# Optimization experiments

Hardware: AMD Instinct MI355X
Metric: run time of the kernel (lower is better)

The kernel has to match this reference:

```python
import jax, jax.numpy as jnp
import numpy as np

N_NODES = 10000
N_EDGES = 100000
DIM = 768
NEG_SLOPE = 0.2  # PyG GATConv default


def gat_conv(x, src, dst, W, att_src, att_dst, bias, num_nodes):
    """Single-head PyG-style GATConv. src/dst already include self-loops."""
    h = x @ W                                  # [N, D]
    a_s = h @ att_src                          # [N]
    a_d = h @ att_dst                          # [N]
    e = jax.nn.leaky_relu(a_s[src] + a_d[dst], NEG_SLOPE)  # [E']
    # segment softmax over edges sharing the same destination node
    m = jax.ops.segment_max(e, dst, num_segments=num_nodes)  # [N]
    e = jnp.exp(e - m[dst])
    denom = jax.ops.segment_sum(e, dst, num_segments=num_nodes)  # [N]
    alpha = e / denom[dst]                     # [E']
    msg = alpha[:, None] * h[src]              # [E', D]
    out = jax.ops.segment_sum(msg, dst, num_segments=num_nodes)  # [N, D]
    return out + bias


def setup_inputs() -> dict:
    key = jax.random.key(0)
    ks = jax.random.split(key, 12)
    s = 1.0 / np.sqrt(DIM)
    inp = {
        "x": jax.random.normal(ks[0], (N_NODES, DIM), dtype=jnp.float32),
        "edge_index": jax.random.randint(ks[1], (2, N_EDGES), 0, N_NODES, dtype=jnp.int64),
        "W1": jax.random.normal(ks[2], (DIM, DIM), dtype=jnp.float32) * s,
        "att_src1": jax.random.normal(ks[3], (DIM,), dtype=jnp.float32) * s,
        "att_dst1": jax.random.normal(ks[4], (DIM,), dtype=jnp.float32) * s,
        "b1": jnp.zeros((DIM,), dtype=jnp.float32),
        "W2": jax.random.normal(ks[5], (DIM, DIM), dtype=jnp.float32) * s,
        "att_src2": jax.random.normal(ks[6], (DIM,), dtype=jnp.float32) * s,
        "att_dst2": jax.random.normal(ks[7], (DIM,), dtype=jnp.float32) * s,
        "b2": jnp.zeros((DIM,), dtype=jnp.float32),
    }
    return inp


def reference(x, edge_index, W1, att_src1, att_dst1, b1, W2, att_src2, att_dst2, b2):
    n = x.shape[0]
    # PyG GATConv default add_self_loops=True
    loops = jnp.arange(n, dtype=edge_index.dtype)
    src = jnp.concatenate([edge_index[0], loops])
    dst = jnp.concatenate([edge_index[1], loops])
    h = gat_conv(x, src, dst, W1, att_src1, att_dst1, b1, n)
    h = jax.nn.relu(h)
    # dropout p=0.0 in eval -> identity
    out = gat_conv(h, src, dst, W2, att_src2, att_dst2, b2, n)
    return out
```

## Files before the change

kernel.cpp:

```cpp
#include <hip/hip_runtime.h>

#define DIM 768
#define NEG_SLOPE 0.2f

typedef unsigned short ushort_t;
typedef short short8 __attribute__((ext_vector_type(8)));
typedef float floatx4 __attribute__((ext_vector_type(4)));

__device__ __forceinline__ ushort_t f32_to_bf16(float f) {
  unsigned int b = __float_as_uint(f);
  b += 0x7FFFu + ((b >> 16) & 1u);
  return (ushort_t)(b >> 16);
}
__device__ __forceinline__ float bf16_to_f32(ushort_t u) {
  return __uint_as_float(((unsigned int)u) << 16);
}
__device__ __forceinline__ float bf16lo(unsigned int u) {
  return __uint_as_float(u << 16);
}
__device__ __forceinline__ float bf16hi(unsigned int u) {
  return __uint_as_float(u & 0xFFFF0000u);
}
__device__ __forceinline__ unsigned int pack_bf16x2(float lo, float hi) {
  return ((unsigned int)f32_to_bf16(lo)) | (((unsigned int)f32_to_bf16(hi)) << 16);
}

__device__ __forceinline__ void gl2lds16(const ushort_t* g, ushort_t* l) {
  __builtin_amdgcn_global_load_lds(
      (const __attribute__((address_space(1))) void*)g,
      (__attribute__((address_space(3))) void*)l, 16, 0, 0);
}

__global__ __launch_bounds__(256)
void prep_kernel(const float* __restrict__ x, ushort_t* __restrict__ xb, int n4,
                 const float* __restrict__ W1, ushort_t* __restrict__ wT1,
                 const float* __restrict__ W2, ushort_t* __restrict__ wT2,
                 int* __restrict__ zbase, int nz) {
  int i = blockIdx.x * 256 + threadIdx.x;
  if (i < n4) {
    float4 v = ((const float4*)x)[i];
    ushort4 o;
    o.x = f32_to_bf16(v.x); o.y = f32_to_bf16(v.y);
    o.z = f32_to_bf16(v.z); o.w = f32_to_bf16(v.w);
    ((ushort4*)xb)[i] = o;
  }
  if (i < DIM * DIM) {
    int nrow = i / DIM;
    int k = i - nrow * DIM;
    wT1[i] = f32_to_bf16(W1[k * DIM + nrow]);
    wT2[i] = f32_to_bf16(W2[k * DIM + nrow]);
  }
  if (i < nz) zbase[i] = 0;
}

__global__ void hist_kernel(const int* __restrict__ ei, int* __restrict__ deg,
                            int E, int Etot) {
  int e = blockIdx.x * 256 + threadIdx.x;
  if (e >= Etot) return;
  int d = (e < E) ? ei[E + e] : (e - E);
  atomicAdd(&deg[d], 1);
}

__global__ __launch_bounds__(256)
void scan_kernel(const int* __restrict__ deg, int* __restrict__ rowstart,
                 int* __restrict__ cursor, int n, int etot) {
  __shared__ int sdeg[10240];
  __shared__ int part[256];
  int tid = threadIdx.x;
  for (int i = tid; i < n; i += 256) sdeg[i] = deg[i];
  __syncthreads();
  int chunk = ((n + 255) / 256) | 1;
  int lo = min(tid * chunk, n);
  int hi = min(lo + chunk, n);
  int s = 0;
  for (int i = lo; i < hi; ++i) s += sdeg[i];
  part[tid] = s;
  __syncthreads();
  for (int off = 1; off < 256; off <<= 1) {
    int v = part[tid];
    int add = (tid >= off) ? part[tid - off] : 0;
    __syncthreads();
    part[tid] = v + add;
    __syncthreads();
  }
  int run = (tid == 0) ? 0 : part[tid - 1];
  for (int i = lo; i < hi; ++i) {
    int d = sdeg[i];
    sdeg[i] = run;
    run += d;
  }
  __syncthreads();
  for (int i = tid; i < n; i += 256) {
    int v = sdeg[i];
    rowstart[i] = v;
    cursor[i] = v;
  }
  if (tid == 0) rowstart[n] = etot;
}

__global__ void fill_kernel(const int* __restrict__ ei, int* __restrict__ cursor,
                            int* __restrict__ col, int E, int Etot) {
  int e = blockIdx.x * 256 + threadIdx.x;
  if (e >= Etot) return;
  int s, d;
  if (e < E) { s = ei[e]; d = ei[E + e]; }
  else       { s = e - E; d = e - E; }
  int pos = atomicAdd(&cursor[d], 1);
  col[pos] = s;
}

__global__ __launch_bounds__(512)
void gemm_kernel(const ushort_t* __restrict__ A, const ushort_t* __restrict__ Bt,
                 const float* __restrict__ att_s, const float* __restrict__ att_d,
                 float* __restrict__ a_s, float* __restrict__ a_d,
                 ushort_t* __restrict__ Hb, int M) {
  const int K = DIM;
  __shared__ __align__(16) ushort_t As[256 * 64];
  __shared__ __align__(16) ushort_t Bs[128 * 64];
  int tid = threadIdx.x;
  int m0 = blockIdx.x * 256, n0 = blockIdx.y * 128;
  int wave = tid >> 6, lane = tid & 63;
  int wm = (wave >> 1) * 64, wn = (wave & 1) * 64;
  int quad = lane >> 4, l16 = lane & 15;

  floatx4 acc[4][4];
  const floatx4 fzero = {0.f, 0.f, 0.f, 0.f};
#pragma unroll
  for (int i = 0; i < 4; ++i)
#pragma unroll
    for (int j = 0; j < 4; ++j) acc[i][j] = fzero;

  int lr = lane >> 3, lc = lane & 7;
  const ushort_t* gA[4];
  const ushort_t* gB[2];
  ushort_t* lA[4];
  ushort_t* lB[2];
#pragma unroll
  for (int t = 0; t < 4; ++t) {
    int r = (wave * 4 + t) * 8 + lr;
    int g = lc ^ (r & 7);
    gA[t] = A + (size_t)min(m0 + r, M - 1) * K + g * 8;
    lA[t] = As + (wave * 4 + t) * 8 * 64;
  }
#pragma unroll
  for (int t = 0; t < 2; ++t) {
    int r = (wave * 2 + t) * 8 + lr;
    int g = lc ^ (r & 7);
    gB[t] = Bt + (size_t)(n0 + r) * K + g * 8;
    lB[t] = Bs + (wave * 2 + t) * 8 * 64;
  }

  for (int k0 = 0; k0 < K; k0 += 64) {
#pragma unroll
    for (int t = 0; t < 4; ++t) gl2lds16(gA[t] + k0, lA[t]);
#pragma unroll
    for (int t = 0; t < 2; ++t) gl2lds16(gB[t] + k0, lB[t]);
    __syncthreads();

#pragma unroll
    for (int h = 0; h < 2; ++h) {
      short8 af[4], bfr[4];
#pragma unroll
      for (int i = 0; i < 4; ++i) {
        int ra = wm + i * 16 + l16;
        af[i] = *(const short8*)(As + ra * 64 + ((((h << 2) | quad)) ^ (ra & 7)) * 8);
        int rb = wn + i * 16 + l16;
        bfr[i] = *(const short8*)(Bs + rb * 64 + ((((h << 2) | quad)) ^ (rb & 7)) * 8);
      }
#pragma unroll
      for (int i = 0; i < 4; ++i)
#pragma unroll
        for (int j = 0; j < 4; ++j)
          acc[i][j] = __builtin_amdgcn_mfma_f32_16x16x32_bf16(af[i], bfr[j], acc[i][j], 0, 0, 0);
    }
    __syncthreads();
  }

  float avs[4], avd[4];
#pragma unroll
  for (int j = 0; j < 4; ++j) {
    int c = n0 + wn + j * 16 + l16;
    avs[j] = att_s[c];
    avd[j] = att_d[c];
  }

#pragma unroll
  for (int i = 0; i < 4; ++i) {
#pragma unroll
    for (int r = 0; r < 4; ++r) {
      int row = m0 + wm + i * 16 + quad * 4 + r;
      bool valid = row < M;
      float pvs = 0.f, pvd = 0.f;
#pragma unroll
      for (int j = 0; j < 4; ++j) {
        float v = acc[i][j][r];
        if (valid) Hb[(size_t)row * DIM + n0 + wn + j * 16 + l16] = f32_to_bf16(v);
        pvs = fmaf(v, avs[j], pvs);
        pvd = fmaf(v, avd[j], pvd);
      }
#pragma unroll
      for (int off = 1; off < 16; off <<= 1) {
        pvs += __shfl_xor(pvs, off, 64);
        pvd += __shfl_xor(pvd, off, 64);
      }
      if (valid && l16 == 0) {
        atomicAdd(a_s + row, pvs);
        atomicAdd(a_d + row, pvd);
      }
    }
  }
}

__global__ __launch_bounds__(256)
void aggregate_kernel(const ushort_t* __restrict__ h, const float* __restrict__ a_s,
                      const float* __restrict__ a_d, const int* __restrict__ rowstart,
                      const int* __restrict__ col, const float* __restrict__ bias,
                      float* __restrict__ out_f32, ushort_t* __restrict__ out_bf16,
                      int relu_mode, int N) {
  int wave = threadIdx.x >> 6, lane = threadIdx.x & 63;
  int node = blockIdx.x * 4 + wave;
  if (node >= N) return;
  int start = rowstart[node], end = rowstart[node + 1];
  float ad = a_d[node];

  float vmax = -3.4e38f;
  for (int e = start + lane; e < end; e += 64) {
    float v = a_s[col[e]] + ad;
    v = (v > 0.f) ? v : NEG_SLOPE * v;
    vmax = fmaxf(vmax, v);
  }
#pragma unroll
  for (int off = 32; off > 0; off >>= 1) vmax = fmaxf(vmax, __shfl_xor(vmax, off, 64));

  float ssum = 0.f;
  for (int e = start + lane; e < end; e += 64) {
    float v = a_s[col[e]] + ad;
    v = (v > 0.f) ? v : NEG_SLOPE * v;
    ssum += __expf(v - vmax);
  }
#pragma unroll
  for (int off = 32; off > 0; off >>= 1) ssum += __shfl_xor(ssum, off, 64);
  float inv = 1.f / ssum;

  float acc8[8];
  float acc4[4];
#pragma unroll
  for (int k = 0; k < 8; ++k) acc8[k] = 0.f;
#pragma unroll
  for (int k = 0; k < 4; ++k) acc4[k] = 0.f;

  for (int base = start; base < end; base += 64) {
    int e = base + lane;
    float al = 0.f;
    int sc = 0;
    if (e < end) {
      sc = col[e];
      float v = a_s[sc] + ad;
      v = (v > 0.f) ? v : NEG_SLOPE * v;
      al = __expf(v - vmax) * inv;
    }
    int cnt = min(64, end - base);
    for (int j = 0; j < cnt; ++j) {
      float w = __shfl(al, j, 64);
      int s = __shfl(sc, j, 64);
      const ushort_t* hr = h + (size_t)s * DIM;
      uint4 u = *(const uint4*)(hr + lane * 8);
      ushort4 t = *(const ushort4*)(hr + 512 + lane * 4);
      acc8[0] = fmaf(w, bf16lo(u.x), acc8[0]);
      acc8[1] = fmaf(w, bf16hi(u.x), acc8[1]);
      acc8[2] = fmaf(w, bf16lo(u.y), acc8[2]);
      acc8[3] = fmaf(w, bf16hi(u.y), acc8[3]);
      acc8[4] = fmaf(w, bf16lo(u.z), acc8[4]);
      acc8[5] = fmaf(w, bf16hi(u.z), acc8[5]);
      acc8[6] = fmaf(w, bf16lo(u.w), acc8[6]);
      acc8[7] = fmaf(w, bf16hi(u.w), acc8[7]);
      acc4[0] = fmaf(w, bf16_to_f32(t.x), acc4[0]);
      acc4[1] = fmaf(w, bf16_to_f32(t.y), acc4[1]);
      acc4[2] = fmaf(w, bf16_to_f32(t.z), acc4[2]);
      acc4[3] = fmaf(w, bf16_to_f32(t.w), acc4[3]);
    }
  }

  size_t ob = (size_t)node * DIM;
  int c8 = lane * 8, c4 = 512 + lane * 4;
  float4 b0 = *(const float4*)(bias + c8);
  float4 b1 = *(const float4*)(bias + c8 + 4);
  float4 b2 = *(const float4*)(bias + c4);
  float o[12];
  o[0] = acc8[0] + b0.x; o[1] = acc8[1] + b0.y;
  o[2] = acc8[2] + b0.z; o[3] = acc8[3] + b0.w;
  o[4] = acc8[4] + b1.x; o[5] = acc8[5] + b1.y;
  o[6] = acc8[6] + b1.z; o[7] = acc8[7] + b1.w;
  o[8] = acc4[0] + b2.x; o[9] = acc4[1] + b2.y;
  o[10] = acc4[2] + b2.z; o[11] = acc4[3] + b2.w;
  if (relu_mode) {
#pragma unroll
    for (int k = 0; k < 12; ++k) o[k] = fmaxf(o[k], 0.f);
    uint4 s0;
    s0.x = pack_bf16x2(o[0], o[1]);
    s0.y = pack_bf16x2(o[2], o[3]);
    s0.z = pack_bf16x2(o[4], o[5]);
    s0.w = pack_bf16x2(o[6], o[7]);
    *(uint4*)(out_bf16 + ob + c8) = s0;
    uint2 s1;
    s1.x = pack_bf16x2(o[8], o[9]);
    s1.y = pack_bf16x2(o[10], o[11]);
    *(uint2*)(out_bf16 + ob + c4) = s1;
  } else {
    *(float4*)(out_f32 + ob + c8) = make_float4(o[0], o[1], o[2], o[3]);
    *(float4*)(out_f32 + ob + c8 + 4) = make_float4(o[4], o[5], o[6], o[7]);
    *(float4*)(out_f32 + ob + c4) = make_float4(o[8], o[9], o[10], o[11]);
  }
}

extern "C" void kernel_launch(void* const* d_in, const int* in_sizes, int n_in,
                              void* d_out, int out_size, void* d_ws, size_t ws_size,
                              hipStream_t stream) {
  const float* x   = (const float*)d_in[0];
  const int*   ei  = (const int*)d_in[1];
  const float* W1  = (const float*)d_in[2];
  const float* as1 = (const float*)d_in[3];
  const float* ad1 = (const float*)d_in[4];
  const float* b1  = (const float*)d_in[5];
  const float* W2  = (const float*)d_in[6];
  const float* as2 = (const float*)d_in[7];
  const float* ad2 = (const float*)d_in[8];
  const float* b2  = (const float*)d_in[9];

  const int N = in_sizes[0] / DIM;
  const int E = in_sizes[1] / 2;
  const int Etot = E + N;

  char* p = (char*)d_ws;
  auto alloc = [&](size_t bytes) {
    char* q = p;
    p += (bytes + 255) & ~(size_t)255;
    return q;
  };
  ushort_t* Hb     = (ushort_t*)alloc((size_t)N * DIM * 2);
  ushort_t* xb     = (ushort_t*)alloc((size_t)N * DIM * 2);
  ushort_t* wT1    = (ushort_t*)alloc((size_t)DIM * DIM * 2);
  ushort_t* wT2    = (ushort_t*)alloc((size_t)DIM * DIM * 2);
  int*      zbase  = (int*)alloc((size_t)5 * N * 4);
  int*      deg    = zbase;
  float*    a_s1   = (float*)(zbase + N);
  float*    a_d1   = (float*)(zbase + 2 * N);
  float*    a_s2   = (float*)(zbase + 3 * N);
  float*    a_d2   = (float*)(zbase + 4 * N);
  int*      rowst  = (int*)alloc((size_t)(N + 1) * 4);
  int*      cursor = (int*)alloc((size_t)N * 4);
  int*      col    = (int*)alloc((size_t)Etot * 4);

  prep_kernel<<<(N * DIM / 4 + 255) / 256, 256, 0, stream>>>(
      x, xb, N * DIM / 4, W1, wT1, W2, wT2, zbase, 5 * N);
  hist_kernel<<<(Etot + 255) / 256, 256, 0, stream>>>(ei, deg, E, Etot);
  scan_kernel<<<1, 256, 0, stream>>>(deg, rowst, cursor, N, Etot);
  fill_kernel<<<(Etot + 255) / 256, 256, 0, stream>>>(ei, cursor, col, E, Etot);

  dim3 ggrid((N + 255) / 256, DIM / 128);

  gemm_kernel<<<ggrid, 512, 0, stream>>>(xb, wT1, as1, ad1, a_s1, a_d1, Hb, N);
  aggregate_kernel<<<(N + 3) / 4, 256, 0, stream>>>(Hb, a_s1, a_d1, rowst, col, b1,
                                                    nullptr, xb, 1, N);
  gemm_kernel<<<ggrid, 512, 0, stream>>>(xb, wT2, as2, ad2, a_s2, a_d2, Hb, N);
  aggregate_kernel<<<(N + 3) / 4, 256, 0, stream>>>(Hb, a_s2, a_d2, rowst, col, b2,
                                                    (float*)d_out, nullptr, 0, N);
}
```

Baseline: 232.9 us.

## Tile weight transpose, widen scan, swizzle GEMM grid, split aggregation into slabs

```diff
diff --git a/kernel.cpp b/kernel.cpp
--- a/kernel.cpp
+++ b/kernel.cpp
@@ -35,22 +35,48 @@
 void prep_kernel(const float* __restrict__ x, ushort_t* __restrict__ xb, int n4,
                  const float* __restrict__ W1, ushort_t* __restrict__ wT1,
                  const float* __restrict__ W2, ushort_t* __restrict__ wT2,
-                 int* __restrict__ zbase, int nz) {
-  int i = blockIdx.x * 256 + threadIdx.x;
-  if (i < n4) {
-    float4 v = ((const float4*)x)[i];
-    ushort4 o;
-    o.x = f32_to_bf16(v.x); o.y = f32_to_bf16(v.y);
-    o.z = f32_to_bf16(v.z); o.w = f32_to_bf16(v.w);
-    ((ushort4*)xb)[i] = o;
-  }
-  if (i < DIM * DIM) {
-    int nrow = i / DIM;
-    int k = i - nrow * DIM;
-    wT1[i] = f32_to_bf16(W1[k * DIM + nrow]);
-    wT2[i] = f32_to_bf16(W2[k * DIM + nrow]);
-  }
-  if (i < nz) zbase[i] = 0;
+                 int* __restrict__ zbase, int nz4) {
+  __shared__ ushort_t tile[64][65];
+  int b = blockIdx.x;
+  int t = threadIdx.x;
+  if (b < 288) {
+    int mat = b / 144;
+    int ti = b - mat * 144;
+    int tr = (ti / 12) * 64;
+    int tc = (ti % 12) * 64;
+    const float* W = mat ? W2 : W1;
+    ushort_t* wT = mat ? wT2 : wT1;
+    int lr = t >> 4, lc4 = (t & 15) * 4;
+#pragma unroll
+    for (int p = 0; p < 4; ++p) {
+      int row = lr + p * 16;
+      float4 v = *(const float4*)(W + (size_t)(tr + row) * DIM + tc + lc4);
+      tile[row][lc4 + 0] = f32_to_bf16(v.x);
+      tile[row][lc4 + 1] = f32_to_bf16(v.y);
+      tile[row][lc4 + 2] = f32_to_bf16(v.z);
+      tile[row][lc4 + 3] = f32_to_bf16(v.w);
+    }
+    __syncthreads();
+    int n = t & 63, kb = (t >> 6) * 16;
+    ushort_t tmp[16];
+#pragma unroll
+    for (int i = 0; i < 16; ++i) tmp[i] = tile[kb + i][n];
+    ushort_t* dst = wT + (size_t)(tc + n) * DIM + tr + kb;
+    *(uint4*)(dst) = *(const uint4*)(&tmp[0]);
+    *(uint4*)(dst + 8) = *(const uint4*)(&tmp[8]);
+  } else {
+    int i = (b - 288) * 256 + t;
+    if (i < n4) {
+      float4 v = ((const float4*)x)[i];
+      ushort4 o;
+      o.x = f32_to_bf16(v.x); o.y = f32_to_bf16(v.y);
+      o.z = f32_to_bf16(v.z); o.w = f32_to_bf16(v.w);
+      ((ushort4*)xb)[i] = o;
+    }
+    if (i < nz4) {
+      ((uint4*)zbase)[i] = make_uint4(0, 0, 0, 0);
+    }
+  }
 }
 
 __global__ void hist_kernel(const int* __restrict__ ei, int* __restrict__ deg,
@@ -61,22 +87,22 @@
   atomicAdd(&deg[d], 1);
 }
 
-__global__ __launch_bounds__(256)
+__global__ __launch_bounds__(1024)
 void scan_kernel(const int* __restrict__ deg, int* __restrict__ rowstart,
                  int* __restrict__ cursor, int n, int etot) {
   __shared__ int sdeg[10240];
-  __shared__ int part[256];
+  __shared__ int part[1024];
   int tid = threadIdx.x;
-  for (int i = tid; i < n; i += 256) sdeg[i] = deg[i];
+  for (int i = tid; i < n; i += 1024) sdeg[i] = deg[i];
   __syncthreads();
-  int chunk = ((n + 255) / 256) | 1;
+  int chunk = ((n + 1023) / 1024) | 1;
   int lo = min(tid * chunk, n);
   int hi = min(lo + chunk, n);
   int s = 0;
   for (int i = lo; i < hi; ++i) s += sdeg[i];
   part[tid] = s;
   __syncthreads();
-  for (int off = 1; off < 256; off <<= 1) {
+  for (int off = 1; off < 1024; off <<= 1) {
     int v = part[tid];
     int add = (tid >= off) ? part[tid - off] : 0;
     __syncthreads();
@@ -90,7 +116,7 @@
     run += d;
   }
   __syncthreads();
-  for (int i = tid; i < n; i += 256) {
+  for (int i = tid; i < n; i += 1024) {
     int v = sdeg[i];
     rowstart[i] = v;
     cursor[i] = v;
@@ -118,7 +144,10 @@
   __shared__ __align__(16) ushort_t As[256 * 64];
   __shared__ __align__(16) ushort_t Bs[128 * 64];
   int tid = threadIdx.x;
-  int m0 = blockIdx.x * 256, n0 = blockIdx.y * 128;
+  int b = blockIdx.x;
+  int g = b / 48, r = b - g * 48;
+  int nblk = r >> 3, mr = r & 7;
+  int m0 = (g * 8 + mr) * 256, n0 = nblk * 128;
   int wave = tid >> 6, lane = tid & 63;
   int wm = (wave >> 1) * 64, wn = (wave & 1) * 64;
   int quad = lane >> 4, l16 = lane & 15;
@@ -137,16 +166,16 @@
   ushort_t* lB[2];
 #pragma unroll
   for (int t = 0; t < 4; ++t) {
-    int r = (wave * 4 + t) * 8 + lr;
-    int g = lc ^ (r & 7);
-    gA[t] = A + (size_t)min(m0 + r, M - 1) * K + g * 8;
+    int rr = (wave * 4 + t) * 8 + lr;
+    int gg = lc ^ (rr & 7);
+    gA[t] = A + (size_t)min(m0 + rr, M - 1) * K + gg * 8;
     lA[t] = As + (wave * 4 + t) * 8 * 64;
   }
 #pragma unroll
   for (int t = 0; t < 2; ++t) {
-    int r = (wave * 2 + t) * 8 + lr;
-    int g = lc ^ (r & 7);
-    gB[t] = Bt + (size_t)(n0 + r) * K + g * 8;
+    int rr = (wave * 2 + t) * 8 + lr;
+    int gg = lc ^ (rr & 7);
+    gB[t] = Bt + (size_t)(n0 + rr) * K + gg * 8;
     lB[t] = Bs + (wave * 2 + t) * 8 * 64;
   }
 
@@ -187,13 +216,13 @@
 #pragma unroll
   for (int i = 0; i < 4; ++i) {
 #pragma unroll
-    for (int r = 0; r < 4; ++r) {
-      int row = m0 + wm + i * 16 + quad * 4 + r;
+    for (int r2 = 0; r2 < 4; ++r2) {
+      int row = m0 + wm + i * 16 + quad * 4 + r2;
       bool valid = row < M;
       float pvs = 0.f, pvd = 0.f;
 #pragma unroll
       for (int j = 0; j < 4; ++j) {
-        float v = acc[i][j][r];
+        float v = acc[i][j][r2];
         if (valid) Hb[(size_t)row * DIM + n0 + wn + j * 16 + l16] = f32_to_bf16(v);
         pvs = fmaf(v, avs[j], pvs);
         pvd = fmaf(v, avd[j], pvd);
@@ -217,8 +246,10 @@
                       const int* __restrict__ col, const float* __restrict__ bias,
                       float* __restrict__ out_f32, ushort_t* __restrict__ out_bf16,
                       int relu_mode, int N) {
+  int slab = blockIdx.x & 7;
+  int grp = blockIdx.x >> 3;
   int wave = threadIdx.x >> 6, lane = threadIdx.x & 63;
-  int node = blockIdx.x * 4 + wave;
+  int node = grp * 4 + wave;
   if (node >= N) return;
   int start = rowstart[node], end = rowstart[node + 1];
   float ad = a_d[node];
@@ -242,12 +273,9 @@
   for (int off = 32; off > 0; off >>= 1) ssum += __shfl_xor(ssum, off, 64);
   float inv = 1.f / ssum;
 
-  float acc8[8];
-  float acc4[4];
-#pragma unroll
-  for (int k = 0; k < 8; ++k) acc8[k] = 0.f;
-#pragma unroll
-  for (int k = 0; k < 4; ++k) acc4[k] = 0.f;
+  float acc0 = 0.f, acc1 = 0.f;
+  const ushort_t* hs = h + slab * 96;
+  bool active = lane < 48;
 
   for (int base = start; base < end; base += 64) {
     int e = base + lane;
@@ -263,53 +291,26 @@
     for (int j = 0; j < cnt; ++j) {
       float w = __shfl(al, j, 64);
       int s = __shfl(sc, j, 64);
-      const ushort_t* hr = h + (size_t)s * DIM;
-      uint4 u = *(const uint4*)(hr + lane * 8);
-      ushort4 t = *(const ushort4*)(hr + 512 + lane * 4);
-      acc8[0] = fmaf(w, bf16lo(u.x), acc8[0]);
-      acc8[1] = fmaf(w, bf16hi(u.x), acc8[1]);
-      acc8[2] = fmaf(w, bf16lo(u.y), acc8[2]);
-      acc8[3] = fmaf(w, bf16hi(u.y), acc8[3]);
-      acc8[4] = fmaf(w, bf16lo(u.z), acc8[4]);
-      acc8[5] = fmaf(w, bf16hi(u.z), acc8[5]);
-      acc8[6] = fmaf(w, bf16lo(u.w), acc8[6]);
-      acc8[7] = fmaf(w, bf16hi(u.w), acc8[7]);
-      acc4[0] = fmaf(w, bf16_to_f32(t.x), acc4[0]);
-      acc4[1] = fmaf(w, bf16_to_f32(t.y), acc4[1]);
-      acc4[2] = fmaf(w, bf16_to_f32(t.z), acc4[2]);
-      acc4[3] = fmaf(w, bf16_to_f32(t.w), acc4[3]);
-    }
-  }
-
-  size_t ob = (size_t)node * DIM;
-  int c8 = lane * 8, c4 = 512 + lane * 4;
-  float4 b0 = *(const float4*)(bias + c8);
-  float4 b1 = *(const float4*)(bias + c8 + 4);
-  float4 b2 = *(const float4*)(bias + c4);
-  float o[12];
-  o[0] = acc8[0] + b0.x; o[1] = acc8[1] + b0.y;
-  o[2] = acc8[2] + b0.z; o[3] = acc8[3] + b0.w;
-  o[4] = acc8[4] + b1.x; o[5] = acc8[5] + b1.y;
-  o[6] = acc8[6] + b1.z; o[7] = acc8[7] + b1.w;
-  o[8] = acc4[0] + b2.x; o[9] = acc4[1] + b2.y;
-  o[10] = acc4[2] + b2.z; o[11] = acc4[3] + b2.w;
-  if (relu_mode) {
-#pragma unroll
-    for (int k = 0; k < 12; ++k) o[k] = fmaxf(o[k], 0.f);
-    uint4 s0;
-    s0.x = pack_bf16x2(o[0], o[1]);
-    s0.y = pack_bf16x2(o[2], o[3]);
-    s0.z = pack_bf16x2(o[4], o[5]);
-    s0.w = pack_bf16x2(o[6], o[7]);
-    *(uint4*)(out_bf16 + ob + c8) = s0;
-    uint2 s1;
-    s1.x = pack_bf16x2(o[8], o[9]);
-    s1.y = pack_bf16x2(o[10], o[11]);
-    *(uint2*)(out_bf16 + ob + c4) = s1;
-  } else {
-    *(float4*)(out_f32 + ob + c8) = make_float4(o[0], o[1], o[2], o[3]);
-    *(float4*)(out_f32 + ob + c8 + 4) = make_float4(o[4], o[5], o[6], o[7]);
-    *(float4*)(out_f32 + ob + c4) = make_float4(o[8], o[9], o[10], o[11]);
+      if (active) {
+        unsigned int u = *(const unsigned int*)(hs + (size_t)s * DIM + lane * 2);
+        acc0 = fmaf(w, bf16lo(u), acc0);
+        acc1 = fmaf(w, bf16hi(u), acc1);
+      }
+    }
+  }
+
+  if (active) {
+    int c = slab * 96 + lane * 2;
+    float2 bv = *(const float2*)(bias + c);
+    float o0 = acc0 + bv.x;
+    float o1 = acc1 + bv.y;
+    if (relu_mode) {
+      o0 = fmaxf(o0, 0.f);
+      o1 = fmaxf(o1, 0.f);
+      *(unsigned int*)(out_bf16 + (size_t)node * DIM + c) = pack_bf16x2(o0, o1);
+    } else {
+      *(float2*)(out_f32 + (size_t)node * DIM + c) = make_float2(o0, o1);
+    }
   }
 }
 
@@ -341,7 +342,7 @@
   ushort_t* xb     = (ushort_t*)alloc((size_t)N * DIM * 2);
   ushort_t* wT1    = (ushort_t*)alloc((size_t)DIM * DIM * 2);
   ushort_t* wT2    = (ushort_t*)alloc((size_t)DIM * DIM * 2);
-  int*      zbase  = (int*)alloc((size_t)5 * N * 4);
+  int*      zbase  = (int*)alloc((size_t)5 * N * 4 + 16);
   int*      deg    = zbase;
   float*    a_s1   = (float*)(zbase + N);
   float*    a_d1   = (float*)(zbase + 2 * N);
@@ -351,18 +352,22 @@
   int*      cursor = (int*)alloc((size_t)N * 4);
   int*      col    = (int*)alloc((size_t)Etot * 4);
 
-  prep_kernel<<<(N * DIM / 4 + 255) / 256, 256, 0, stream>>>(
-      x, xb, N * DIM / 4, W1, wT1, W2, wT2, zbase, 5 * N);
+  int n4 = N * DIM / 4;
+  int nz4 = (5 * N + 3) / 4;
+  int prep_blocks = 288 + (n4 + 255) / 256;
+  prep_kernel<<<prep_blocks, 256, 0, stream>>>(x, xb, n4, W1, wT1, W2, wT2,
+                                               zbase, nz4);
   hist_kernel<<<(Etot + 255) / 256, 256, 0, stream>>>(ei, deg, E, Etot);
-  scan_kernel<<<1, 256, 0, stream>>>(deg, rowst, cursor, N, Etot);
+  scan_kernel<<<1, 1024, 0, stream>>>(deg, rowst, cursor, N, Etot);
   fill_kernel<<<(Etot + 255) / 256, 256, 0, stream>>>(ei, cursor, col, E, Etot);
 
-  dim3 ggrid((N + 255) / 256, DIM / 128);
-
-  gemm_kernel<<<ggrid, 512, 0, stream>>>(xb, wT1, as1, ad1, a_s1, a_d1, Hb, N);
-  aggregate_kernel<<<(N + 3) / 4, 256, 0, stream>>>(Hb, a_s1, a_d1, rowst, col, b1,
-                                                    nullptr, xb, 1, N);
-  gemm_kernel<<<ggrid, 512, 0, stream>>>(xb, wT2, as2, ad2, a_s2, a_d2, Hb, N);
-  aggregate_kernel<<<(N + 3) / 4, 256, 0, stream>>>(Hb, a_s2, a_d2, rowst, col, b2,
-                                                    (float*)d_out, nullptr, 0, N);
-}
+  int gemm_blocks = ((N + 255) / 256) * 6 * 8 / 8;
+  int agg_blocks = ((N + 3) / 4) * 8;
+
+  gemm_kernel<<<gemm_blocks, 512, 0, stream>>>(xb, wT1, as1, ad1, a_s1, a_d1, Hb, N);
+  aggregate_kernel<<<agg_blocks, 256, 0, stream>>>(Hb, a_s1, a_d1, rowst, col, b1,
+                                                   nullptr, xb, 1, N);
+  gemm_kernel<<<gemm_blocks, 512, 0, stream>>>(xb, wT2, as2, ad2, a_s2, a_d2, Hb, N);
+  aggregate_kernel<<<agg_blocks, 256, 0, stream>>>(Hb, a_s2, a_d2, rowst, col, b2,
+                                                   (float*)d_out, nullptr, 0, N);
+}
```

Result: slower. 308.6 us (+32.5%).
